# Kernel tuning notes

Measured on AMD Instinct MI355X. Metric: run time of the kernel, lower is better.

The kernel has to match this reference:

```python
import jax, jax.numpy as jnp
import numpy as np


def setup_inputs() -> dict:
    key = jax.random.key(0)
    k1, k2 = jax.random.split(key)
    queries = jax.random.normal(k1, (16, 1024, 256), dtype=jnp.float32)
    embedding = jax.random.normal(k2, (8192, 256), dtype=jnp.float32) * 0.02
    return {"queries": queries, "embedding": embedding}


def reference(queries, embedding):
    commitment_weight = 0.25
    # squared L2 distances: ||q||^2 + ||e||^2 - 2 q.e  -> [b, k, n]
    q_sq = jnp.sum(queries * queries, axis=-1, keepdims=True)          # [b,k,1]
    e_sq = jnp.sum(embedding * embedding, axis=-1)[None, None, :]      # [1,1,n]
    distances = q_sq + e_sq - 2.0 * jnp.einsum('bkc,nc->bkn', queries, embedding)
    code_indices = jnp.argmin(distances, axis=-1)                      # [b,k] int
    quantized = embedding[code_indices]                                # [b,k,c]
    commit_loss = jnp.mean((jax.lax.stop_gradient(queries) - quantized) ** 2)
    codebook_loss = jnp.mean((queries - jax.lax.stop_gradient(quantized)) ** 2)
    vq_loss = codebook_loss + commitment_weight * commit_loss
    # straight-through estimator
    quantized_st = queries + jax.lax.stop_gradient(quantized - queries)
    return (code_indices, quantized_st, vq_loss)
```

## Files before the change

kernel.cpp:

```cpp
#include <hip/hip_runtime.h>
#include <float.h>

typedef _Float16 half8 __attribute__((ext_vector_type(8)));
typedef _Float16 half4v __attribute__((ext_vector_type(4)));
typedef float f32x4 __attribute__((ext_vector_type(4)));

#define M_TOTAL 16384
#define N_CODES 8192
#define KDIM    256
#define BM 128
#define BN 256
#define BK 32
#define NK (KDIM / BK)
#define NB (N_CODES / BN)
#define TS 32
#define MARGIN 3.6e-3f
#define SQ_SCALE 512.0f
#define SE_SCALE 2048.0f
#define INV_PROD 1.9073486328125e-06f
#define RG 4
#define RCODES 1024
#define RNCH (N_CODES / RCODES)
#define RPB 1024
#define RM_BLOCKS 256
#define LR_BLOCKS 32

#define PREP_Q_BLOCKS (M_TOTAL / 4)
#define PREP_E_BLOCKS (N_CODES / 4)
#define TR_BLOCKS ((N_CODES / 64) * (KDIM / 64))

__device__ __forceinline__ void prep_body(const float* __restrict__ src,
                                          _Float16* __restrict__ dst,
                                          float* __restrict__ sq, float scale,
                                          int row0, int tid) {
    {
        const int r = row0 + (tid >> 6);
        const int e4 = tid & 63;
        const float4 v = *(const float4*)(src + (size_t)r * KDIM + e4 * 4);
        const half4v h = {(_Float16)(v.x * scale), (_Float16)(v.y * scale),
                          (_Float16)(v.z * scale), (_Float16)(v.w * scale)};
        ((half4v*)(dst + (size_t)r * KDIM))[e4] = h;
    }
    if (tid < 64) {
        const int grp = tid >> 4;
        const int sub = tid & 15;
        const int row = row0 + grp;
        const float* p = src + (size_t)row * KDIM + (sub >> 3) * 128 + (sub & 7);
        float r;
        {
            #pragma clang fp contract(off)
            float v = p[0];
            r = v * v;
            #pragma unroll
            for (int k = 1; k < 16; k++) { const float w = p[k * 8]; r = r + w * w; }
        }
        const float t1 = r  + __shfl_xor(r,  1, 64);
        const float t2 = t1 + __shfl_xor(t1, 2, 64);
        const float t3 = t2 + __shfl_xor(t2, 4, 64);
        const float t4 = t3 + __shfl_xor(t3, 8, 64);
        if (sub == 0) sq[row] = t4;
    }
}

__global__ void prep_fused_kernel(const float* __restrict__ Q, const float* __restrict__ E,
                                  _Float16* __restrict__ Qh, _Float16* __restrict__ Eh,
                                  float* __restrict__ qsq, float* __restrict__ esq,
                                  float* __restrict__ ET,
                                  int* __restrict__ fcount, float* __restrict__ loss_slot) {
    __shared__ float tile[64][65];
    const int tid = threadIdx.x;
    const int b = blockIdx.x;
    if (b == 0 && tid == 0) { *fcount = 0; *loss_slot = 0.f; }
    if (b < PREP_Q_BLOCKS) {
        prep_body(Q, Qh, qsq, SQ_SCALE, b * 4, tid);
        return;
    }
    if (b < PREP_Q_BLOCKS + PREP_E_BLOCKS) {
        prep_body(E, Eh, esq, SE_SCALE, (b - PREP_Q_BLOCKS) * 4, tid);
        return;
    }
    const int idx = b - PREP_Q_BLOCKS - PREP_E_BLOCKS;
    const int n0 = (idx & 127) * 64;
    const int k0 = (idx >> 7) * 64;
    const int r = tid >> 4;
    const int c4 = tid & 15;
    #pragma unroll
    for (int p = 0; p < 4; p++) {
        const int row = p * 16 + r;
        const float4 v = *(const float4*)(E + (size_t)(n0 + row) * KDIM + k0 + c4 * 4);
        tile[row][c4 * 4 + 0] = v.x;
        tile[row][c4 * 4 + 1] = v.y;
        tile[row][c4 * 4 + 2] = v.z;
        tile[row][c4 * 4 + 3] = v.w;
    }
    __syncthreads();
    #pragma unroll
    for (int p = 0; p < 4; p++) {
        const int d = p * 16 + r;
        float4 o;
        o.x = tile[c4 * 4 + 0][d];
        o.y = tile[c4 * 4 + 1][d];
        o.z = tile[c4 * 4 + 2][d];
        o.w = tile[c4 * 4 + 3][d];
        *(float4*)(ET + (size_t)(k0 + d) * N_CODES + n0 + c4 * 4) = o;
    }
}

union SMemU {
    struct { _Float16 q[3][BM * TS]; _Float16 e[3][BN * TS]; } t;
    struct { unsigned k1[BM][2]; unsigned k2[BM][2]; } red;
};

__device__ __forceinline__ void gl_lds16(const void* g, void* lds) {
    __builtin_amdgcn_global_load_lds(
        (const __attribute__((address_space(1))) unsigned*)g,
        (__attribute__((address_space(3))) unsigned*)lds, 16, 0, 0);
}

__global__ __launch_bounds__(256, 2)
void mfma_top2_kernel(const _Float16* __restrict__ Qh, const _Float16* __restrict__ Eh,
                      const float* __restrict__ esq,
                      unsigned* __restrict__ k1s, unsigned* __restrict__ k2s) {
    __shared__ SMemU sm;
    const int tid = threadIdx.x;
    const int m0 = blockIdx.x * BM;
    const int n0 = blockIdx.y * BN;
    const int w = tid >> 6, lane = tid & 63;
    const int wm = w >> 1, wn = w & 1;
    const int qd = lane >> 4, c = lane & 15;

    const int lrow = lane >> 2;
    const int gsw = (lane & 3) ^ ((lane >> 3) & 3);
    const _Float16* qsrc = Qh + (size_t)(m0 + w * 32 + lrow) * KDIM + gsw * 8;
    const _Float16* esrc = Eh + (size_t)(n0 + w * 64 + lrow) * KDIM + gsw * 8;

    f32x4 acc[4][8];
    const f32x4 zero = {0.f, 0.f, 0.f, 0.f};
    #pragma unroll
    for (int mt = 0; mt < 4; mt++)
        #pragma unroll
        for (int nt = 0; nt < 8; nt++) acc[mt][nt] = zero;

    #define STAGE(buf, kofs) do {                                                  \
        _Float16* qdst = sm.t.q[buf] + w * 1024;                                   \
        _Float16* edst = sm.t.e[buf] + w * 2048;                                   \
        gl_lds16(qsrc + (kofs),             qdst);                                 \
        gl_lds16(qsrc + 16 * KDIM + (kofs), qdst + 512);                           \
        gl_lds16(esrc + (kofs),             edst);                                 \
        gl_lds16(esrc + 16 * KDIM + (kofs), edst + 512);                           \
        gl_lds16(esrc + 32 * KDIM + (kofs), edst + 1024);                          \
        gl_lds16(esrc + 48 * KDIM + (kofs), edst + 1536);                          \
    } while (0)

    STAGE(0, 0);
    STAGE(1, BK);
    STAGE(2, 2 * BK);

    float es8[8];
    #pragma unroll
    for (int nt = 0; nt < 8; nt++) es8[nt] = esq[n0 + wn * 128 + nt * 16 + c] + 8.0f;

    asm volatile("s_waitcnt vmcnt(12)" ::: "memory");
    __builtin_amdgcn_s_barrier();

    const int csw = (c >> 1) & 3;

    #pragma unroll
    for (int ki = 0; ki < NK; ki++) {
        const int buf = ki % 3;
        const _Float16* bq = sm.t.q[buf];
        const _Float16* be = sm.t.e[buf];

        half8 qa[4];
        #pragma unroll
        for (int mt = 0; mt < 4; mt++)
            qa[mt] = *(const half8*)(bq + (wm * 64 + mt * 16 + c) * TS + (qd ^ csw) * 8);
        half8 eh[4];
        #pragma unroll
        for (int nt = 0; nt < 4; nt++)
            eh[nt] = *(const half8*)(be + (wn * 128 + nt * 16 + c) * TS + (qd ^ csw) * 8);
        __builtin_amdgcn_s_barrier();
        __builtin_amdgcn_s_setprio(1);
        #pragma unroll
        for (int nt = 0; nt < 4; nt++)
            #pragma unroll
            for (int mt = 0; mt < 4; mt++)
                acc[mt][nt] = __builtin_amdgcn_mfma_f32_16x16x32_f16(qa[mt], eh[nt], acc[mt][nt], 0, 0, 0);
        __builtin_amdgcn_s_setprio(0);

        half8 eh2[4];
        #pragma unroll
        for (int nt = 0; nt < 4; nt++)
            eh2[nt] = *(const half8*)(be + (wn * 128 + (nt + 4) * 16 + c) * TS + (qd ^ csw) * 8);
        __builtin_amdgcn_s_barrier();
        __builtin_amdgcn_s_setprio(1);
        #pragma unroll
        for (int nt = 0; nt < 4; nt++)
            #pragma unroll
            for (int mt = 0; mt < 4; mt++)
                acc[mt][nt + 4] = __builtin_amdgcn_mfma_f32_16x16x32_f16(qa[mt], eh2[nt], acc[mt][nt + 4], 0, 0, 0);
        __builtin_amdgcn_s_setprio(0);

        if (ki == NK - 1) break;
        if (ki <= NK - 3) { asm volatile("s_waitcnt vmcnt(6)" ::: "memory"); }
        else              { asm volatile("s_waitcnt vmcnt(0)" ::: "memory"); }
        __builtin_amdgcn_s_barrier();
        if (ki + 3 < NK) STAGE(buf, (ki + 3) * BK);
    }
    #undef STAGE

    unsigned k1[16], k2[16];
    #pragma unroll
    for (int i = 0; i < 16; i++) { k1[i] = 0xFFFFFFFFu; k2[i] = 0xFFFFFFFFu; }

    #pragma unroll
    for (int mt = 0; mt < 4; mt++)
        #pragma unroll
        for (int nt = 0; nt < 8; nt++) {
            const unsigned nl = (unsigned)(wn * 128 + nt * 16 + c);
            #pragma unroll
            for (int r = 0; r < 4; r++) {
                const int i = mt * 4 + r;
                const float d = fmaf(acc[mt][nt][r], -INV_PROD, es8[nt]);
                const unsigned k = (__float_as_uint(d) & 0xFFFFFF00u) | nl;
                const unsigned t = min(k1[i], k);
                k2[i] = min(k2[i], max(k1[i], k));
                k1[i] = t;
            }
        }
    #pragma unroll
    for (int s = 1; s < 16; s <<= 1) {
        #pragma unroll
        for (int i = 0; i < 16; i++) {
            const unsigned ok1 = (unsigned)__shfl_xor((int)k1[i], s, 64);
            const unsigned ok2 = (unsigned)__shfl_xor((int)k2[i], s, 64);
            const unsigned t = min(k1[i], ok1);
            k2[i] = min(min(k2[i], ok2), max(k1[i], ok1));
            k1[i] = t;
        }
    }
    __syncthreads();
    if (c == 0) {
        #pragma unroll
        for (int mt = 0; mt < 4; mt++)
            #pragma unroll
            for (int r = 0; r < 4; r++) {
                const int ml = wm * 64 + mt * 16 + qd * 4 + r;
                sm.red.k1[ml][wn] = k1[mt * 4 + r];
                sm.red.k2[ml][wn] = k2[mt * 4 + r];
            }
    }
    __syncthreads();
    if (tid < BM) {
        const unsigned a1 = sm.red.k1[tid][0], b1 = sm.red.k1[tid][1];
        const unsigned a2 = sm.red.k2[tid][0], b2 = sm.red.k2[tid][1];
        const size_t o = (size_t)(m0 + tid) * NB + blockIdx.y;
        k1s[o] = min(a1, b1);
        k2s[o] = min(min(a2, b2), max(a1, b1));
    }
}

__global__ void finalize_kernel(const float* __restrict__ Q, const float* __restrict__ E,
                                const unsigned* __restrict__ k1s, const unsigned* __restrict__ k2s,
                                int* __restrict__ fcount, int* __restrict__ flist,
                                float* __restrict__ ws_loss, float* __restrict__ out) {
    const int q = blockIdx.x * 4 + (threadIdx.x >> 6);
    const int lane = threadIdx.x & 63;
    unsigned d1 = 0xFFFFFF00u;
    unsigned d2 = 0xFFFFFF00u;
    int gi = 0x7FFFFFFF;
    if (lane < NB) {
        const unsigned k1 = k1s[(size_t)q * NB + lane];
        const unsigned k2 = k2s[(size_t)q * NB + lane];
        d1 = k1 & 0xFFFFFF00u;
        gi = lane * BN + (int)(k1 & 255u);
        d2 = k2 & 0xFFFFFF00u;
    }
    #pragma unroll
    for (int s = 1; s < 64; s <<= 1) {
        const unsigned od1 = (unsigned)__shfl_xor((int)d1, s, 64);
        const int      ogi = __shfl_xor(gi, s, 64);
        const unsigned od2 = (unsigned)__shfl_xor((int)d2, s, 64);
        const unsigned nd2 = min(min(d2, od2), max(d1, od1));
        const bool take = (od1 < d1) || (od1 == d1 && ogi < gi);
        d1 = take ? od1 : d1;
        gi = take ? ogi : gi;
        d2 = nd2;
    }
    if ((__uint_as_float(d2) - __uint_as_float(d1)) < MARGIN) {
        if (lane == 0) flist[atomicAdd(fcount, 1)] = q;
        return;
    }

    if (lane == 0) out[q] = (float)gi;
    const float4 qv = *(const float4*)(Q + (size_t)q * KDIM + lane * 4);
    const float4 ev = *(const float4*)(E + (size_t)gi * KDIM + lane * 4);
    float4 st;
    {
        #pragma clang fp contract(off)
        st.x = qv.x + (ev.x - qv.x);
        st.y = qv.y + (ev.y - qv.y);
        st.z = qv.z + (ev.z - qv.z);
        st.w = qv.w + (ev.w - qv.w);
    }
    *(float4*)(out + M_TOTAL + (size_t)q * KDIM + lane * 4) = st;

    const float dx = qv.x - ev.x, dy = qv.y - ev.y, dz = qv.z - ev.z, dw = qv.w - ev.w;
    float s = dx * dx + dy * dy + dz * dz + dw * dw;
    #pragma unroll
    for (int off = 32; off > 0; off >>= 1) s += __shfl_down(s, off);
    if (lane == 0) ws_loss[q] = s;
}

__global__ __launch_bounds__(256, 4)
void refine_partial_kernel(const float* __restrict__ Q, const float* __restrict__ ET,
                           const float* __restrict__ qsq, const float* __restrict__ esq,
                           const int* __restrict__ fcount, const int* __restrict__ flist,
                           float* __restrict__ rp_v, int* __restrict__ rp_i) {
    const int cnt = *fcount;
    if (cnt == 0) return;
    const int ngroups = (cnt + RG - 1) / RG;
    const int ntasks = ngroups * RNCH;
    const int tid = threadIdx.x;
    const int w = tid >> 6, lane = tid & 63;
    __shared__ float qs[RG][KDIM];
    __shared__ float redv[4][RG];
    __shared__ int   redi[4][RG];

    for (int t = blockIdx.x; t < ntasks; t += RPB) {
        const int grp = t >> 3;
        const int chunk = t & (RNCH - 1);
        __syncthreads();
        {
            const int g = tid >> 6, c4 = tid & 63;
            const int fi = min(grp * RG + g, cnt - 1);
            const int q = flist[fi];
            *(float4*)&qs[g][c4 * 4] = *(const float4*)(Q + (size_t)q * KDIM + c4 * 4);
        }
        __syncthreads();

        const int nb = chunk * RCODES + tid * 4;
        float a[RG][4];
        #pragma unroll
        for (int g = 0; g < RG; g++)
            #pragma unroll
            for (int j = 0; j < 4; j++) a[g][j] = 0.f;

        for (int k4 = 0; k4 < KDIM / 4; k4++) {
            float4 qv[RG];
            #pragma unroll
            for (int g = 0; g < RG; g++) qv[g] = *(const float4*)&qs[g][k4 * 4];
            #pragma unroll
            for (int kk = 0; kk < 4; kk++) {
                const float4 ev = *(const float4*)(ET + (size_t)(k4 * 4 + kk) * N_CODES + nb);
                #pragma unroll
                for (int g = 0; g < RG; g++) {
                    const float qk = (kk == 0) ? qv[g].x : (kk == 1) ? qv[g].y
                                   : (kk == 2) ? qv[g].z : qv[g].w;
                    a[g][0] = fmaf(qk, ev.x, a[g][0]);
                    a[g][1] = fmaf(qk, ev.y, a[g][1]);
                    a[g][2] = fmaf(qk, ev.z, a[g][2]);
                    a[g][3] = fmaf(qk, ev.w, a[g][3]);
                }
            }
        }

        float es[4];
        #pragma unroll
        for (int j = 0; j < 4; j++) es[j] = esq[nb + j];

        #pragma unroll
        for (int g = 0; g < RG; g++) {
            const int fi = min(grp * RG + g, cnt - 1);
            const float qsv = qsq[flist[fi]];
            float bv = FLT_MAX; int bi = 0x7fffffff;
            #pragma unroll
            for (int j = 0; j < 4; j++) {
                float d;
                {
                    #pragma clang fp contract(off)
                    const float t1 = qsv + es[j];
                    d = t1 - 2.0f * a[g][j];
                }
                if (d < bv) { bv = d; bi = nb + j; }
            }
            #pragma unroll
            for (int s = 1; s < 64; s <<= 1) {
                const float ov = __shfl_xor(bv, s, 64);
                const int   oi = __shfl_xor(bi, s, 64);
                if (ov < bv || (ov == bv && oi < bi)) { bv = ov; bi = oi; }
            }
            if (lane == 0) { redv[w][g] = bv; redi[w][g] = bi; }
        }
        __syncthreads();
        if (tid < RG) {
            float fv = redv[0][tid]; int fidx = redi[0][tid];
            #pragma unroll
            for (int u = 1; u < 4; u++) {
                if (redv[u][tid] < fv || (redv[u][tid] == fv && redi[u][tid] < fidx)) {
                    fv = redv[u][tid]; fidx = redi[u][tid];
                }
            }
            rp_v[(size_t)t * RG + tid] = fv;
            rp_i[(size_t)t * RG + tid] = fidx;
        }
    }
}

__global__ void refine_merge_kernel(const float* __restrict__ Q, const float* __restrict__ E,
                                    const int* __restrict__ fcount, const int* __restrict__ flist,
                                    const float* __restrict__ rp_v, const int* __restrict__ rp_i,
                                    float* __restrict__ ws_loss, float* __restrict__ out) {
    const int cnt = *fcount;
    const int lane = threadIdx.x;
    for (int fi = blockIdx.x; fi < cnt; fi += RM_BLOCKS) {
        const int q = flist[fi];
        const int grp = fi >> 2, g = fi & 3;
        float bv = FLT_MAX; int bi = 0x7fffffff;
        if (lane < RNCH) {
            const size_t t = (size_t)(grp * RNCH + lane);
            bv = rp_v[t * RG + g];
            bi = rp_i[t * RG + g];
        }
        #pragma unroll
        for (int s = 1; s < 64; s <<= 1) {
            const float ov = __shfl_xor(bv, s, 64);
            const int   oi = __shfl_xor(bi, s, 64);
            if (ov < bv || (ov == bv && oi < bi)) { bv = ov; bi = oi; }
        }
        if (lane == 0) out[q] = (float)bi;

        const float4 qv = *(const float4*)(Q + (size_t)q * KDIM + lane * 4);
        const float4 ev = *(const float4*)(E + (size_t)bi * KDIM + lane * 4);
        float4 st;
        {
            #pragma clang fp contract(off)
            st.x = qv.x + (ev.x - qv.x);
            st.y = qv.y + (ev.y - qv.y);
            st.z = qv.z + (ev.z - qv.z);
            st.w = qv.w + (ev.w - qv.w);
        }
        *(float4*)(out + M_TOTAL + (size_t)q * KDIM + lane * 4) = st;
        const float dx = qv.x - ev.x, dy = qv.y - ev.y, dz = qv.z - ev.z, dw = qv.w - ev.w;
        float s = dx * dx + dy * dy + dz * dz + dw * dw;
        #pragma unroll
        for (int off = 32; off > 0; off >>= 1) s += __shfl_down(s, off);
        if (lane == 0) ws_loss[q] = s;
    }
}

__global__ void loss_reduce_kernel(const float* __restrict__ ws_loss, float* __restrict__ out) {
    const int tid = threadIdx.x;
    float s = 0.f;
    for (int i = blockIdx.x * 256 + tid; i < M_TOTAL; i += LR_BLOCKS * 256)
        s += ws_loss[i];
    #pragma unroll
    for (int off = 32; off > 0; off >>= 1) s += __shfl_down(s, off);
    __shared__ float ws[4];
    if ((tid & 63) == 0) ws[tid >> 6] = s;
    __syncthreads();
    if (tid == 0) {
        const float tot = (ws[0] + ws[1]) + (ws[2] + ws[3]);
        atomicAdd(out + M_TOTAL + (size_t)M_TOTAL * KDIM,
                  tot * (1.25f / (float)((size_t)M_TOTAL * KDIM)));
    }
}

extern "C" void kernel_launch(void* const* d_in, const int* in_sizes, int n_in,
                              void* d_out, int out_size, void* d_ws, size_t ws_size,
                              hipStream_t stream) {
    const float* Q = (const float*)d_in[0];
    const float* E = (const float*)d_in[1];
    float* out = (float*)d_out;

    char* ws = (char*)d_ws;
    _Float16* Qh  = (_Float16*)(ws);
    _Float16* Eh  = (_Float16*)(ws + (size_t)8  * 1024 * 1024);
    float* qsq    = (float*)   (ws + (size_t)12 * 1024 * 1024);
    float* esq    = qsq + M_TOTAL;
    unsigned* k1s = (unsigned*)(ws + (size_t)13 * 1024 * 1024);
    unsigned* k2s = (unsigned*)(ws + (size_t)17 * 1024 * 1024);
    int*   fcount = (int*)     (ws + (size_t)25 * 1024 * 1024);
    int*   flist  = fcount + 64;
    float* ws_loss= (float*)   (ws + (size_t)25 * 1024 * 1024 + 512 * 1024);
    float* ET     = (float*)   (ws + (size_t)26 * 1024 * 1024);
    float* rp_v   = (float*)k1s;
    int*   rp_i   = (int*)k2s;
    float* loss_slot = out + M_TOTAL + (size_t)M_TOTAL * KDIM;

    prep_fused_kernel<<<PREP_Q_BLOCKS + PREP_E_BLOCKS + TR_BLOCKS, 256, 0, stream>>>(
        Q, E, Qh, Eh, qsq, esq, ET, fcount, loss_slot);

    mfma_top2_kernel<<<dim3(M_TOTAL / BM, N_CODES / BN), 256, 0, stream>>>(
        Qh, Eh, esq, k1s, k2s);

    finalize_kernel<<<M_TOTAL / 4, 256, 0, stream>>>(Q, E, k1s, k2s, fcount, flist, ws_loss, out);
    refine_partial_kernel<<<RPB, 256, 0, stream>>>(Q, ET, qsq, esq, fcount, flist, rp_v, rp_i);
    refine_merge_kernel<<<RM_BLOCKS, 64, 0, stream>>>(Q, E, fcount, flist, rp_v, rp_i, ws_loss, out);
    loss_reduce_kernel<<<LR_BLOCKS, 256, 0, stream>>>(ws_loss, out);
}
```

Measured before the change: 226.8 us.

## Enlarge GEMM tile to 256x256 with 8 waves and split staging

The distance GEMM block grows from 128x256 with 4 waves to 256x256 with 8 waves in a 2x4 layout. This raises operand reuse per LDS byte and halves the number of query blocks. The prefetch schedule changes from three stages issued after the barrier to two-ahead staging, with A and B loads interleaved between the two MFMA halves. The cross-wave top-2 reduction now merges four column partitions. The trade-off is a larger LDS footprint (about 96KB), which may cut occupancy to one block per CU, plus more registers per wave.

```diff
diff --git a/kernel.cpp b/kernel.cpp
--- a/kernel.cpp
+++ b/kernel.cpp
@@ -8,10 +8,10 @@
 #define M_TOTAL 16384
 #define N_CODES 8192
 #define KDIM    256
-#define BM 128
+#define BM 256
 #define BN 256
 #define BK 32
-#define NK (KDIM / BK)
+#define NKS (KDIM / BK)
 #define NB (N_CODES / BN)
 #define TS 32
 #define MARGIN 3.6e-3f
@@ -107,8 +107,8 @@
 }
 
 union SMemU {
-    struct { _Float16 q[3][BM * TS]; _Float16 e[3][BN * TS]; } t;
-    struct { unsigned k1[BM][2]; unsigned k2[BM][2]; } red;
+    struct { _Float16 a[3][BM * TS]; _Float16 b[3][BN * TS]; } t;
+    struct { unsigned k1[BM][4]; unsigned k2[BM][4]; } red;
 };
 
 __device__ __forceinline__ void gl_lds16(const void* g, void* lds) {
@@ -117,7 +117,7 @@
         (__attribute__((address_space(3))) unsigned*)lds, 16, 0, 0);
 }
 
-__global__ __launch_bounds__(256, 2)
+__global__ __launch_bounds__(512, 2)
 void mfma_top2_kernel(const _Float16* __restrict__ Qh, const _Float16* __restrict__ Eh,
                       const float* __restrict__ esq,
                       unsigned* __restrict__ k1s, unsigned* __restrict__ k2s) {
@@ -126,98 +126,99 @@
     const int m0 = blockIdx.x * BM;
     const int n0 = blockIdx.y * BN;
     const int w = tid >> 6, lane = tid & 63;
-    const int wm = w >> 1, wn = w & 1;
+    const int wm = w >> 2, wn = w & 3;
     const int qd = lane >> 4, c = lane & 15;
 
     const int lrow = lane >> 2;
     const int gsw = (lane & 3) ^ ((lane >> 3) & 3);
-    const _Float16* qsrc = Qh + (size_t)(m0 + w * 32 + lrow) * KDIM + gsw * 8;
-    const _Float16* esrc = Eh + (size_t)(n0 + w * 64 + lrow) * KDIM + gsw * 8;
-
-    f32x4 acc[4][8];
+    const _Float16* qsrcA = Qh + (size_t)(m0 + w * 16 + lrow) * KDIM + gsw * 8;
+    const _Float16* esrcB = Eh + (size_t)(n0 + w * 16 + lrow) * KDIM + gsw * 8;
+
+    float es8[4];
+    #pragma unroll
+    for (int nt = 0; nt < 4; nt++) es8[nt] = esq[n0 + wn * 64 + nt * 16 + c] + 8.0f;
+
+    f32x4 acc[8][4];
     const f32x4 zero = {0.f, 0.f, 0.f, 0.f};
     #pragma unroll
-    for (int mt = 0; mt < 4; mt++)
-        #pragma unroll
-        for (int nt = 0; nt < 8; nt++) acc[mt][nt] = zero;
-
-    #define STAGE(buf, kofs) do {                                                  \
-        _Float16* qdst = sm.t.q[buf] + w * 1024;                                   \
-        _Float16* edst = sm.t.e[buf] + w * 2048;                                   \
-        gl_lds16(qsrc + (kofs),             qdst);                                 \
-        gl_lds16(qsrc + 16 * KDIM + (kofs), qdst + 512);                           \
-        gl_lds16(esrc + (kofs),             edst);                                 \
-        gl_lds16(esrc + 16 * KDIM + (kofs), edst + 512);                           \
-        gl_lds16(esrc + 32 * KDIM + (kofs), edst + 1024);                          \
-        gl_lds16(esrc + 48 * KDIM + (kofs), edst + 1536);                          \
+    for (int mt = 0; mt < 8; mt++)
+        #pragma unroll
+        for (int nt = 0; nt < 4; nt++) acc[mt][nt] = zero;
+
+    #define STAGE_A(buf, ks) do {                                                  \
+        _Float16* d0 = sm.t.a[buf] + w * 512;                                      \
+        const _Float16* s0 = qsrcA + (ks) * BK;                                    \
+        gl_lds16(s0,              d0);                                             \
+        gl_lds16(s0 + 128 * KDIM, d0 + 4096);                                      \
     } while (0)
-
-    STAGE(0, 0);
-    STAGE(1, BK);
-    STAGE(2, 2 * BK);
-
-    float es8[8];
-    #pragma unroll
-    for (int nt = 0; nt < 8; nt++) es8[nt] = esq[n0 + wn * 128 + nt * 16 + c] + 8.0f;
-
-    asm volatile("s_waitcnt vmcnt(12)" ::: "memory");
+    #define STAGE_B(buf, ks) do {                                                  \
+        _Float16* d0 = sm.t.b[buf] + w * 512;                                      \
+        const _Float16* s0 = esrcB + (ks) * BK;                                    \
+        gl_lds16(s0,              d0);                                             \
+        gl_lds16(s0 + 128 * KDIM, d0 + 4096);                                      \
+    } while (0)
+
+    STAGE_A(0, 0); STAGE_B(0, 0);
+    STAGE_A(1, 1); STAGE_B(1, 1);
+    asm volatile("s_waitcnt vmcnt(4)" ::: "memory");
     __builtin_amdgcn_s_barrier();
 
     const int csw = (c >> 1) & 3;
 
     #pragma unroll
-    for (int ki = 0; ki < NK; ki++) {
+    for (int ki = 0; ki < NKS; ki++) {
         const int buf = ki % 3;
-        const _Float16* bq = sm.t.q[buf];
-        const _Float16* be = sm.t.e[buf];
-
-        half8 qa[4];
+        const _Float16* ba = sm.t.a[buf];
+        const _Float16* bb = sm.t.b[buf];
+
+        half8 qa[4], eb[4];
         #pragma unroll
         for (int mt = 0; mt < 4; mt++)
-            qa[mt] = *(const half8*)(bq + (wm * 64 + mt * 16 + c) * TS + (qd ^ csw) * 8);
-        half8 eh[4];
+            qa[mt] = *(const half8*)(ba + (wm * 128 + mt * 16 + c) * TS + (qd ^ csw) * 8);
         #pragma unroll
         for (int nt = 0; nt < 4; nt++)
-            eh[nt] = *(const half8*)(be + (wn * 128 + nt * 16 + c) * TS + (qd ^ csw) * 8);
+            eb[nt] = *(const half8*)(bb + (wn * 64 + nt * 16 + c) * TS + (qd ^ csw) * 8);
+        if (ki + 2 < NKS) STAGE_A((ki + 2) % 3, ki + 2);
         __builtin_amdgcn_s_barrier();
         __builtin_amdgcn_s_setprio(1);
         #pragma unroll
         for (int nt = 0; nt < 4; nt++)
             #pragma unroll
             for (int mt = 0; mt < 4; mt++)
-                acc[mt][nt] = __builtin_amdgcn_mfma_f32_16x16x32_f16(qa[mt], eh[nt], acc[mt][nt], 0, 0, 0);
+                acc[mt][nt] = __builtin_amdgcn_mfma_f32_16x16x32_f16(qa[mt], eb[nt], acc[mt][nt], 0, 0, 0);
         __builtin_amdgcn_s_setprio(0);
 
-        half8 eh2[4];
-        #pragma unroll
-        for (int nt = 0; nt < 4; nt++)
-            eh2[nt] = *(const half8*)(be + (wn * 128 + (nt + 4) * 16 + c) * TS + (qd ^ csw) * 8);
+        half8 qb[4];
+        #pragma unroll
+        for (int mt = 0; mt < 4; mt++)
+            qb[mt] = *(const half8*)(ba + (wm * 128 + (mt + 4) * 16 + c) * TS + (qd ^ csw) * 8);
+        if (ki + 2 < NKS) STAGE_B((ki + 2) % 3, ki + 2);
         __builtin_amdgcn_s_barrier();
         __builtin_amdgcn_s_setprio(1);
         #pragma unroll
         for (int nt = 0; nt < 4; nt++)
             #pragma unroll
             for (int mt = 0; mt < 4; mt++)
-                acc[mt][nt + 4] = __builtin_amdgcn_mfma_f32_16x16x32_f16(qa[mt], eh2[nt], acc[mt][nt + 4], 0, 0, 0);
+                acc[mt + 4][nt] = __builtin_amdgcn_mfma_f32_16x16x32_f16(qb[mt], eb[nt], acc[mt + 4][nt], 0, 0, 0);
         __builtin_amdgcn_s_setprio(0);
 
-        if (ki == NK - 1) break;
-        if (ki <= NK - 3) { asm volatile("s_waitcnt vmcnt(6)" ::: "memory"); }
-        else              { asm volatile("s_waitcnt vmcnt(0)" ::: "memory"); }
+        if (ki == NKS - 1) break;
+        if (ki <= NKS - 3) { asm volatile("s_waitcnt vmcnt(4)" ::: "memory"); }
+        else               { asm volatile("s_waitcnt vmcnt(0)" ::: "memory"); }
         __builtin_amdgcn_s_barrier();
-        if (ki + 3 < NK) STAGE(buf, (ki + 3) * BK);
-    }
-    #undef STAGE
-
-    unsigned k1[16], k2[16];
-    #pragma unroll
-    for (int i = 0; i < 16; i++) { k1[i] = 0xFFFFFFFFu; k2[i] = 0xFFFFFFFFu; }
-
-    #pragma unroll
-    for (int mt = 0; mt < 4; mt++)
-        #pragma unroll
-        for (int nt = 0; nt < 8; nt++) {
-            const unsigned nl = (unsigned)(wn * 128 + nt * 16 + c);
+    }
+    #undef STAGE_A
+    #undef STAGE_B
+
+    unsigned k1[32], k2[32];
+    #pragma unroll
+    for (int i = 0; i < 32; i++) { k1[i] = 0xFFFFFFFFu; k2[i] = 0xFFFFFFFFu; }
+
+    #pragma unroll
+    for (int mt = 0; mt < 8; mt++)
+        #pragma unroll
+        for (int nt = 0; nt < 4; nt++) {
+            const unsigned nl = (unsigned)(wn * 64 + nt * 16 + c);
             #pragma unroll
             for (int r = 0; r < 4; r++) {
                 const int i = mt * 4 + r;
@@ -231,7 +232,7 @@
     #pragma unroll
     for (int s = 1; s < 16; s <<= 1) {
         #pragma unroll
-        for (int i = 0; i < 16; i++) {
+        for (int i = 0; i < 32; i++) {
             const unsigned ok1 = (unsigned)__shfl_xor((int)k1[i], s, 64);
             const unsigned ok2 = (unsigned)__shfl_xor((int)k2[i], s, 64);
             const unsigned t = min(k1[i], ok1);
@@ -242,21 +243,26 @@
     __syncthreads();
     if (c == 0) {
         #pragma unroll
-        for (int mt = 0; mt < 4; mt++)
+        for (int mt = 0; mt < 8; mt++)
             #pragma unroll
             for (int r = 0; r < 4; r++) {
-                const int ml = wm * 64 + mt * 16 + qd * 4 + r;
+                const int ml = wm * 128 + mt * 16 + qd * 4 + r;
                 sm.red.k1[ml][wn] = k1[mt * 4 + r];
                 sm.red.k2[ml][wn] = k2[mt * 4 + r];
             }
     }
     __syncthreads();
     if (tid < BM) {
-        const unsigned a1 = sm.red.k1[tid][0], b1 = sm.red.k1[tid][1];
-        const unsigned a2 = sm.red.k2[tid][0], b2 = sm.red.k2[tid][1];
+        unsigned m1 = sm.red.k1[tid][0], m2 = sm.red.k2[tid][0];
+        #pragma unroll
+        for (int u = 1; u < 4; u++) {
+            const unsigned x1 = sm.red.k1[tid][u], x2 = sm.red.k2[tid][u];
+            m2 = min(min(m2, x2), max(m1, x1));
+            m1 = min(m1, x1);
+        }
         const size_t o = (size_t)(m0 + tid) * NB + blockIdx.y;
-        k1s[o] = min(a1, b1);
-        k2s[o] = min(min(a2, b2), max(a1, b1));
+        k1s[o] = m1;
+        k2s[o] = m2;
     }
 }
 
@@ -491,7 +497,7 @@
     prep_fused_kernel<<<PREP_Q_BLOCKS + PREP_E_BLOCKS + TR_BLOCKS, 256, 0, stream>>>(
         Q, E, Qh, Eh, qsq, esq, ET, fcount, loss_slot);
 
-    mfma_top2_kernel<<<dim3(M_TOTAL / BM, N_CODES / BN), 256, 0, stream>>>(
+    mfma_top2_kernel<<<dim3(M_TOTAL / BM, N_CODES / BN), 512, 0, stream>>>(
         Qh, Eh, esq, k1s, k2s);
 
     finalize_kernel<<<M_TOTAL / 4, 256, 0, stream>>>(Q, E, k1s, k2s, fcount, flist, ws_loss, out);
```

Measured after the change: 262.4 us. +15.7%, slower.
